# Kernel optimization log

Measured on AMD Instinct MI355X. Metric: run time of the kernel, lower is better.

Reference implementation:

```python
import jax, jax.numpy as jnp
import numpy as np

BATCH = 1048576
D_IN = 4        # d_in=3 spatial dims + 1 time dim
HID = 64
N_HID_STACK = 4  # hidden residual blocks after the first hidden layer
D_OUT = 3
BN_EPS = 1e-5


def _bn(x, gamma, beta):
    # BatchNorm1d in training mode: biased batch statistics over the batch axis
    mu = jnp.mean(x, axis=0)
    var = jnp.var(x, axis=0)
    return gamma * (x - mu) * jax.lax.rsqrt(var + BN_EPS) + beta


def setup_inputs() -> dict:
    key = jax.random.key(0)
    ks = jax.random.split(key, 8)
    s_in = 1.0 / np.sqrt(D_IN)
    s_h = 1.0 / np.sqrt(HID)
    return {
        "x": jax.random.normal(ks[0], (BATCH, D_IN), dtype=jnp.float32),
        "bn0_gamma": jnp.ones((D_IN,), jnp.float32),
        "bn0_beta": jnp.zeros((D_IN,), jnp.float32),
        "W0": jax.random.normal(ks[1], (D_IN, HID), jnp.float32) * s_in,
        "b0": jnp.zeros((HID,), jnp.float32),
        "gamma0": jnp.ones((HID,), jnp.float32),
        "beta0": jnp.zeros((HID,), jnp.float32),
        "W_hid": jax.random.normal(ks[2], (N_HID_STACK, HID, HID), jnp.float32) * s_h,
        "b_hid": jnp.zeros((N_HID_STACK, HID), jnp.float32),
        "gamma_hid": jnp.ones((N_HID_STACK, HID), jnp.float32),
        "beta_hid": jnp.zeros((N_HID_STACK, HID), jnp.float32),
        "Wout": jax.random.normal(ks[3], (HID, D_OUT), jnp.float32) * s_h,
        "bout": jnp.zeros((D_OUT,), jnp.float32),
    }


def reference(x, bn0_gamma, bn0_beta, W0, b0, gamma0, beta0,
              W_hid, b_hid, gamma_hid, beta_hid, Wout, bout):
    # Net.forward (u-network, single patch, batch_normalization=True, tanh):
    #   x = bn0(x)
    #   y = bn(act(Linear0(x)))                 (first hidden layer, no skip)
    #   y = bn_i(act(Linear_i(y))) + y          (residual hidden layers)
    #   y = Linear_out(y)
    h = _bn(x, bn0_gamma, bn0_beta)
    y = _bn(jnp.tanh(h @ W0 + b0), gamma0, beta0)

    def step(y, layer):
        W, b, g, be = layer
        return _bn(jnp.tanh(y @ W + b), g, be) + y, None

    y, _ = jax.lax.scan(step, y, (W_hid, b_hid, gamma_hid, beta_hid))
    return y @ Wout + bout
```

## Files before the change

kernel.cpp:

```cpp
#include <hip/hip_runtime.h>
#include <stdint.h>


#define NROWS 1048576
#define EPS 1e-5f
#define INV_B 9.5367431640625e-07f
#define LOG2E2 2.885390081777927f
#define BIGGRID 16384
#define NBUCKET 256

typedef __attribute__((ext_vector_type(8))) short bfrag;
typedef __attribute__((ext_vector_type(4))) float facc;
typedef __attribute__((ext_vector_type(4))) float f4v;

__device__ __forceinline__ float bf2f(short s) {
  union { unsigned u; float f; } v;
  v.u = ((unsigned)(unsigned short)s) << 16;
  return v.f;
}
__device__ __forceinline__ short f2bf(float f) {
  union { float f; unsigned u; } v;
  v.f = f;
  unsigned r = v.u + 0x7FFFu + ((v.u >> 16) & 1u);
  return (short)(r >> 16);
}
__device__ __forceinline__ float tanh_fast(float x) {
  float e = __builtin_amdgcn_exp2f(x * LOG2E2);
  return 1.f - 2.f * __builtin_amdgcn_rcpf(e + 1.f);
}

template <int W>
__global__ __launch_bounds__(256) void k_reduce(const float* __restrict__ P,
                                                float* __restrict__ S,
                                                int rows_per_blk) {
  __shared__ float red[256];
  const int tid = threadIdx.x;
  const int col = tid % W;
  const int grp = tid / W;
  const int G = 256 / W;
  size_t r0 = (size_t)blockIdx.x * rows_per_blk;
  float s = 0.f;
  for (int r = grp; r < rows_per_blk; r += G) s += P[(r0 + r) * W + col];
  red[tid] = s;
  __syncthreads();
  if (tid < W) {
    float t = 0.f;
#pragma unroll 4
    for (int g = 0; g < G; ++g) t += red[g * W + tid];
    atomicAdd(&S[tid], t);
  }
}


__global__ __launch_bounds__(256) void k_stats_x(const float* __restrict__ x,
                                                 float* __restrict__ P) {
  __shared__ float red[4][8];
  const int tid = threadIdx.x;
  const int wave = tid >> 6;
  size_t base = (size_t)blockIdx.x * 1024 + tid;
  float s[4] = {0.f, 0.f, 0.f, 0.f}, q[4] = {0.f, 0.f, 0.f, 0.f};
#pragma unroll
  for (int it = 0; it < 4; ++it) {
    f4v v = *(const f4v*)(x + (base + (size_t)it * 256) * 4);
#pragma unroll
    for (int k = 0; k < 4; ++k) { s[k] += v[k]; q[k] = fmaf(v[k], v[k], q[k]); }
  }
#pragma unroll
  for (int off = 32; off > 0; off >>= 1) {
#pragma unroll
    for (int k = 0; k < 4; ++k) {
      s[k] += __shfl_xor(s[k], off);
      q[k] += __shfl_xor(q[k], off);
    }
  }
  if ((tid & 63) == 0) {
#pragma unroll
    for (int k = 0; k < 4; ++k) { red[wave][k] = s[k]; red[wave][4 + k] = q[k]; }
  }
  __syncthreads();
  if (tid < 8)
    P[blockIdx.x * 8 + tid] =
        red[0][tid] + red[1][tid] + red[2][tid] + red[3][tid];
}

__global__ __launch_bounds__(256) void k_stats_z1(
    const float* __restrict__ x, const float* __restrict__ bn0g,
    const float* __restrict__ bn0b, const float* __restrict__ W0,
    const float* __restrict__ b0, const float* __restrict__ sx,
    float* __restrict__ P) {
  __shared__ float red[2][4][64];
  const int tid = threadIdx.x;
  const int lane = tid & 63;
  const int wave = tid >> 6;
  int gw = blockIdx.x * 4 + wave;
  float sc[4], sh[4];
#pragma unroll
  for (int k = 0; k < 4; ++k) {
    float mean = sx[k] * INV_B;
    float var = fmaf(-mean, mean, sx[4 + k] * INV_B);
    float rs = rsqrtf(var + EPS);
    sc[k] = bn0g[k] * rs;
    sh[k] = fmaf(-sc[k], mean, bn0b[k]);
  }
  float w2[4];
  float b2 = b0[lane];
#pragma unroll
  for (int k = 0; k < 4; ++k) {
    float w = W0[k * 64 + lane];
    w2[k] = sc[k] * w;
    b2 = fmaf(sh[k], w, b2);
  }
  float s = 0.f, q = 0.f;
  size_t r0 = (size_t)gw * 256;
  for (int r = 0; r < 256; ++r) {
    f4v xv = *(const f4v*)(x + (r0 + r) * 4);
    float acc = b2;
#pragma unroll
    for (int k = 0; k < 4; ++k) acc = fmaf(xv[k], w2[k], acc);
    float z = tanh_fast(acc);
    s += z;
    q = fmaf(z, z, q);
  }
  red[0][wave][lane] = s;
  red[1][wave][lane] = q;
  __syncthreads();
  if (tid < 128) {
    int which = tid >> 6, c = tid & 63;
    P[blockIdx.x * 128 + tid] = red[which][0][c] + red[which][1][c] +
                                red[which][2][c] + red[which][3][c];
  }
}

__global__ __launch_bounds__(256) void k_prep(const float* __restrict__ Wh,
                                              short* __restrict__ WT) {
  int idx = blockIdx.x * 256 + threadIdx.x;
  int l = idx >> 12, rem = idx & 4095, k = rem >> 6, c = rem & 63;
  WT[l * 4096 + c * 64 + k] = f2bf(Wh[l * 4096 + k * 64 + c]);
}


__global__ __launch_bounds__(128) void k_first(
    const float* __restrict__ x, const float* __restrict__ bn0g,
    const float* __restrict__ bn0b, const float* __restrict__ W0,
    const float* __restrict__ b0, const float* __restrict__ gamma0,
    const float* __restrict__ beta0, const float* __restrict__ sx,
    const float* __restrict__ s1, const short* __restrict__ WTb,
    const float* __restrict__ bb, float* __restrict__ Pb,
    short* __restrict__ Y) {
  __shared__ __align__(16) float lds_x[64 * 4];
  __shared__ __align__(16) short lds_y[64 * 72];
  __shared__ float lds_st[128];

  const int tid = threadIdx.x;
  const int lane = tid & 63;
  const int wave = tid >> 6;
  const int l15 = lane & 15;
  const int q = lane >> 4;
  const int wr = wave * 32;
  const size_t r0 = (size_t)blockIdx.x * 64;

  f4v xp;
  if (lane < 32) xp = *(const f4v*)(x + (r0 + wr + lane) * 4);

  lds_st[tid] = 0.f;
  float sc0[4], sh0[4];
#pragma unroll
  for (int k = 0; k < 4; ++k) {
    float mean = sx[k] * INV_B;
    float var = fmaf(-mean, mean, sx[4 + k] * INV_B);
    float rs = rsqrtf(var + EPS);
    sc0[k] = bn0g[k] * rs;
    sh0[k] = fmaf(-sc0[k], mean, bn0b[k]);
  }
  float w2[4];
  float b2 = b0[lane];
#pragma unroll
  for (int k = 0; k < 4; ++k) {
    float w = W0[k * 64 + lane];
    w2[k] = sc0[k] * w;
    b2 = fmaf(sh0[k], w, b2);
  }
  float mean1 = s1[lane] * INV_B;
  float var1 = fmaf(-mean1, mean1, s1[64 + lane] * INV_B);
  float A1c = gamma0[lane] * rsqrtf(var1 + EPS);
  float B1c = fmaf(-A1c, mean1, beta0[lane]);
  if (lane < 32) *(f4v*)&lds_x[(wr + lane) * 4] = xp;
  __syncthreads();

  for (int e = 0; e < 32; ++e) {
    int row = wr + e;
    f4v xv = *(const f4v*)&lds_x[row * 4];
    float acc = b2;
#pragma unroll
    for (int k = 0; k < 4; ++k) acc = fmaf(xv[k], w2[k], acc);
    float z = tanh_fast(acc);
    lds_y[row * 72 + lane] = f2bf(fmaf(A1c, z, B1c));
  }

  bfrag af[2][2];
#pragma unroll
  for (int mt = 0; mt < 2; ++mt)
#pragma unroll
    for (int kt = 0; kt < 2; ++kt) {
      af[mt][kt] =
          *(const bfrag*)&lds_y[(wr + mt * 16 + l15) * 72 + kt * 32 + q * 8];
      *(bfrag*)(Y + (r0 + wr + mt * 16 + l15) * 64 + kt * 32 + q * 8) =
          af[mt][kt];
    }
  float bbv[4];
  bfrag bwb[4][2];
#pragma unroll
  for (int nt = 0; nt < 4; ++nt) {
    bbv[nt] = bb[nt * 16 + l15];
#pragma unroll
    for (int kt = 0; kt < 2; ++kt)
      bwb[nt][kt] =
          *(const bfrag*)(WTb + (nt * 16 + l15) * 64 + kt * 32 + q * 8);
  }
  facc acc2[2][4];
#pragma unroll
  for (int mt = 0; mt < 2; ++mt)
#pragma unroll
    for (int nt = 0; nt < 4; ++nt) {
      acc2[mt][nt][0] = bbv[nt]; acc2[mt][nt][1] = bbv[nt];
      acc2[mt][nt][2] = bbv[nt]; acc2[mt][nt][3] = bbv[nt];
    }
#pragma unroll
  for (int mt = 0; mt < 2; ++mt)
#pragma unroll
    for (int nt = 0; nt < 4; ++nt)
#pragma unroll
      for (int kt = 0; kt < 2; ++kt)
        acc2[mt][nt] = __builtin_amdgcn_mfma_f32_16x16x32_bf16(
            af[mt][kt], bwb[nt][kt], acc2[mt][nt], 0, 0, 0);
  float sAcc[4], qAcc[4];
#pragma unroll
  for (int nt = 0; nt < 4; ++nt) {
    sAcc[nt] = 0.f;
    qAcc[nt] = 0.f;
#pragma unroll
    for (int mt = 0; mt < 2; ++mt)
#pragma unroll
      for (int i = 0; i < 4; ++i) {
        float z = tanh_fast(acc2[mt][nt][i]);
        sAcc[nt] += z;
        qAcc[nt] = fmaf(z, z, qAcc[nt]);
      }
    float s = sAcc[nt], ss = qAcc[nt];
    s += __shfl_xor(s, 16); s += __shfl_xor(s, 32);
    ss += __shfl_xor(ss, 16); ss += __shfl_xor(ss, 32);
    if (q == 0) {
      atomicAdd(&lds_st[nt * 16 + l15], s);
      atomicAdd(&lds_st[64 + nt * 16 + l15], ss);
    }
  }
  __syncthreads();
  atomicAdd(&Pb[(size_t)(blockIdx.x & (NBUCKET - 1)) * 128 + tid],
            lds_st[tid]);
}

__global__ __launch_bounds__(128) void k_mid(
    short* __restrict__ Y, const short* __restrict__ WTa,
    const float* __restrict__ ba, const float* __restrict__ ga,
    const float* __restrict__ bea, const float* __restrict__ sa,
    const short* __restrict__ WTb, const float* __restrict__ bb,
    float* __restrict__ Pb) {
  __shared__ __align__(16) short lds_y[64 * 72];
  __shared__ float red[2][128];

  const int tid = threadIdx.x;
  const int lane = tid & 63;
  const int wave = tid >> 6;
  const int l15 = lane & 15;
  const int q = lane >> 4;
  const int wr = wave * 32;
  const size_t r0 = (size_t)blockIdx.x * 64;

  bfrag af[2][2];
#pragma unroll
  for (int mt = 0; mt < 2; ++mt)
#pragma unroll
    for (int kt = 0; kt < 2; ++kt)
      af[mt][kt] =
          *(const bfrag*)(Y + (r0 + wr + mt * 16 + l15) * 64 + kt * 32 + q * 8);

  float Av[4], Bv[4], bav[4];
#pragma unroll
  for (int nt = 0; nt < 4; ++nt) {
    int c = nt * 16 + l15;
    float mean = sa[c] * INV_B;
    float var = fmaf(-mean, mean, sa[64 + c] * INV_B);
    float A = ga[c] * rsqrtf(var + EPS);
    Av[nt] = A;
    Bv[nt] = fmaf(-A, mean, bea[c]);
    bav[nt] = ba[c];
  }
  bfrag bwa[4][2];
#pragma unroll
  for (int nt = 0; nt < 4; ++nt)
#pragma unroll
    for (int kt = 0; kt < 2; ++kt)
      bwa[nt][kt] =
          *(const bfrag*)(WTa + (nt * 16 + l15) * 64 + kt * 32 + q * 8);

#pragma unroll
  for (int mt = 0; mt < 2; ++mt)
#pragma unroll
    for (int kt = 0; kt < 2; ++kt)
      *(bfrag*)&lds_y[(wr + mt * 16 + l15) * 72 + kt * 32 + q * 8] =
          af[mt][kt];

  facc acc[2][4];
#pragma unroll
  for (int mt = 0; mt < 2; ++mt)
#pragma unroll
    for (int nt = 0; nt < 4; ++nt) {
      acc[mt][nt][0] = bav[nt]; acc[mt][nt][1] = bav[nt];
      acc[mt][nt][2] = bav[nt]; acc[mt][nt][3] = bav[nt];
    }
#pragma unroll
  for (int mt = 0; mt < 2; ++mt)
#pragma unroll
    for (int nt = 0; nt < 4; ++nt)
#pragma unroll
      for (int kt = 0; kt < 2; ++kt)
        acc[mt][nt] = __builtin_amdgcn_mfma_f32_16x16x32_bf16(
            af[mt][kt], bwa[nt][kt], acc[mt][nt], 0, 0, 0);

#pragma unroll
  for (int mt = 0; mt < 2; ++mt)
#pragma unroll
    for (int nt = 0; nt < 4; ++nt) {
      int c = nt * 16 + l15;
      float A = Av[nt], Bc = Bv[nt];
#pragma unroll
      for (int i = 0; i < 4; ++i) {
        int rl = wr + mt * 16 + q * 4 + i;
        float z = tanh_fast(acc[mt][nt][i]);
        float yo = bf2f(lds_y[rl * 72 + c]);
        lds_y[rl * 72 + c] = f2bf(fmaf(A, z, Bc) + yo);
      }
    }

#pragma unroll
  for (int mt = 0; mt < 2; ++mt)
#pragma unroll
    for (int kt = 0; kt < 2; ++kt) {
      af[mt][kt] =
          *(const bfrag*)&lds_y[(wr + mt * 16 + l15) * 72 + kt * 32 + q * 8];
      *(bfrag*)(Y + (r0 + wr + mt * 16 + l15) * 64 + kt * 32 + q * 8) =
          af[mt][kt];
    }
  float bbv[4];
  bfrag bwb[4][2];
#pragma unroll
  for (int nt = 0; nt < 4; ++nt) {
    bbv[nt] = bb[nt * 16 + l15];
#pragma unroll
    for (int kt = 0; kt < 2; ++kt)
      bwb[nt][kt] =
          *(const bfrag*)(WTb + (nt * 16 + l15) * 64 + kt * 32 + q * 8);
  }
#pragma unroll
  for (int mt = 0; mt < 2; ++mt)
#pragma unroll
    for (int nt = 0; nt < 4; ++nt) {
      acc[mt][nt][0] = bbv[nt]; acc[mt][nt][1] = bbv[nt];
      acc[mt][nt][2] = bbv[nt]; acc[mt][nt][3] = bbv[nt];
    }
#pragma unroll
  for (int mt = 0; mt < 2; ++mt)
#pragma unroll
    for (int nt = 0; nt < 4; ++nt)
#pragma unroll
      for (int kt = 0; kt < 2; ++kt)
        acc[mt][nt] = __builtin_amdgcn_mfma_f32_16x16x32_bf16(
            af[mt][kt], bwb[nt][kt], acc[mt][nt], 0, 0, 0);
#pragma unroll
  for (int nt = 0; nt < 4; ++nt) {
    float s = 0.f, ss = 0.f;
#pragma unroll
    for (int mt = 0; mt < 2; ++mt)
#pragma unroll
      for (int i = 0; i < 4; ++i) {
        float z = tanh_fast(acc[mt][nt][i]);
        s += z;
        ss = fmaf(z, z, ss);
      }
    s += __shfl_xor(s, 16); s += __shfl_xor(s, 32);
    ss += __shfl_xor(ss, 16); ss += __shfl_xor(ss, 32);
    if (q == 0) {
      red[wave][nt * 16 + l15] = s;
      red[wave][64 + nt * 16 + l15] = ss;
    }
  }
  __syncthreads();
  atomicAdd(&Pb[(size_t)(blockIdx.x & (NBUCKET - 1)) * 128 + tid],
            red[0][tid] + red[1][tid]);
}

__global__ __launch_bounds__(128) void k_last(
    const short* __restrict__ Y, const short* __restrict__ WTa,
    const float* __restrict__ ba, const float* __restrict__ ga,
    const float* __restrict__ bea, const float* __restrict__ sa,
    const float* __restrict__ Wout, const float* __restrict__ bout,
    float* __restrict__ out) {
  __shared__ __align__(16) short lds_y[64 * 72];
  __shared__ float lds_wo[192];

  const int tid = threadIdx.x;
  const int lane = tid & 63;
  const int wave = tid >> 6;
  const int l15 = lane & 15;
  const int q = lane >> 4;
  const int wr = wave * 32;
  const size_t r0 = (size_t)blockIdx.x * 64;

  bfrag af[2][2];
#pragma unroll
  for (int mt = 0; mt < 2; ++mt)
#pragma unroll
    for (int kt = 0; kt < 2; ++kt)
      af[mt][kt] =
          *(const bfrag*)(Y + (r0 + wr + mt * 16 + l15) * 64 + kt * 32 + q * 8);

  for (int i = tid; i < 192; i += 128) lds_wo[i] = Wout[i];
  float Av[4], Bv[4], bav[4];
#pragma unroll
  for (int nt = 0; nt < 4; ++nt) {
    int c = nt * 16 + l15;
    float mean = sa[c] * INV_B;
    float var = fmaf(-mean, mean, sa[64 + c] * INV_B);
    float A = ga[c] * rsqrtf(var + EPS);
    Av[nt] = A;
    Bv[nt] = fmaf(-A, mean, bea[c]);
    bav[nt] = ba[c];
  }
  bfrag bwa[4][2];
#pragma unroll
  for (int nt = 0; nt < 4; ++nt)
#pragma unroll
    for (int kt = 0; kt < 2; ++kt)
      bwa[nt][kt] =
          *(const bfrag*)(WTa + (nt * 16 + l15) * 64 + kt * 32 + q * 8);
  float bo0 = bout[0], bo1 = bout[1], bo2 = bout[2];

#pragma unroll
  for (int mt = 0; mt < 2; ++mt)
#pragma unroll
    for (int kt = 0; kt < 2; ++kt)
      *(bfrag*)&lds_y[(wr + mt * 16 + l15) * 72 + kt * 32 + q * 8] =
          af[mt][kt];
  __syncthreads();

  facc acc[2][4];
#pragma unroll
  for (int mt = 0; mt < 2; ++mt)
#pragma unroll
    for (int nt = 0; nt < 4; ++nt) {
      acc[mt][nt][0] = bav[nt]; acc[mt][nt][1] = bav[nt];
      acc[mt][nt][2] = bav[nt]; acc[mt][nt][3] = bav[nt];
    }
#pragma unroll
  for (int mt = 0; mt < 2; ++mt)
#pragma unroll
    for (int nt = 0; nt < 4; ++nt)
#pragma unroll
      for (int kt = 0; kt < 2; ++kt)
        acc[mt][nt] = __builtin_amdgcn_mfma_f32_16x16x32_bf16(
            af[mt][kt], bwa[nt][kt], acc[mt][nt], 0, 0, 0);
#pragma unroll
  for (int mt = 0; mt < 2; ++mt)
#pragma unroll
    for (int nt = 0; nt < 4; ++nt) {
      int c = nt * 16 + l15;
      float A = Av[nt], Bc = Bv[nt];
#pragma unroll
      for (int i = 0; i < 4; ++i) {
        int rl = wr + mt * 16 + q * 4 + i;
        float z = tanh_fast(acc[mt][nt][i]);
        float yo = bf2f(lds_y[rl * 72 + c]);
        lds_y[rl * 72 + c] = f2bf(fmaf(A, z, Bc) + yo);
      }
    }

  {
    int row = wr + (lane >> 1);
    int cb = (lane & 1) * 32;
    float o0 = 0.f, o1 = 0.f, o2 = 0.f;
#pragma unroll
    for (int jc = 0; jc < 4; ++jc) {
      bfrag v = *(const bfrag*)&lds_y[row * 72 + cb + jc * 8];
#pragma unroll
      for (int j = 0; j < 8; ++j) {
        float f = bf2f(v[j]);
        int jj = cb + jc * 8 + j;
        o0 = fmaf(f, lds_wo[jj * 3 + 0], o0);
        o1 = fmaf(f, lds_wo[jj * 3 + 1], o1);
        o2 = fmaf(f, lds_wo[jj * 3 + 2], o2);
      }
    }
    o0 += __shfl_xor(o0, 1);
    o1 += __shfl_xor(o1, 1);
    o2 += __shfl_xor(o2, 1);
    if ((lane & 1) == 0) {
      size_t ro = (r0 + row) * 3;
      out[ro] = o0 + bo0;
      out[ro + 1] = o1 + bo1;
      out[ro + 2] = o2 + bo2;
    }
  }
}

extern "C" void kernel_launch(void* const* d_in, const int* in_sizes, int n_in,
                              void* d_out, int out_size, void* d_ws,
                              size_t ws_size, hipStream_t stream) {
  (void)in_sizes; (void)n_in; (void)out_size; (void)ws_size;
  const float* x = (const float*)d_in[0];
  const float* bn0g = (const float*)d_in[1];
  const float* bn0b = (const float*)d_in[2];
  const float* W0 = (const float*)d_in[3];
  const float* b0 = (const float*)d_in[4];
  const float* gamma0 = (const float*)d_in[5];
  const float* beta0 = (const float*)d_in[6];
  const float* Wh = (const float*)d_in[7];
  const float* bh = (const float*)d_in[8];
  const float* gh = (const float*)d_in[9];
  const float* beh = (const float*)d_in[10];
  const float* Wout = (const float*)d_in[11];
  const float* bout = (const float*)d_in[12];
  float* out = (float*)d_out;

  char* ws = (char*)d_ws;
  short* Y = (short*)ws;
  const size_t YB = (size_t)NROWS * 64 * 2;
  float* stats = (float*)(ws + YB);
  float* Sx = stats;
  float* S1 = stats + 8;
  float* S2 = stats + 136;
  float* S3 = stats + 264;
  float* S4 = stats + 392;
  float* S5 = stats + 520;
  short* WT = (short*)(ws + YB + 4096);
  float* P = (float*)(ws + YB + 4096 + 32768);
  float* Pb = (float*)(ws + YB + 4096 + 32768 + (1 << 20));
  float* Pb2 = Pb;
  float* Pb3 = Pb + NBUCKET * 128;
  float* Pb4 = Pb + 2 * NBUCKET * 128;
  float* Pb5 = Pb + 3 * NBUCKET * 128;

  hipMemsetAsync(stats, 0, 648 * sizeof(float), stream);
  hipMemsetAsync(Pb, 0, 4 * NBUCKET * 128 * sizeof(float), stream);
  k_prep<<<64, 256, 0, stream>>>(Wh, WT);
  k_stats_x<<<1024, 256, 0, stream>>>(x, P);
  k_reduce<8><<<8, 256, 0, stream>>>(P, Sx, 128);
  k_stats_z1<<<1024, 256, 0, stream>>>(x, bn0g, bn0b, W0, b0, Sx, P);
  k_reduce<128><<<8, 256, 0, stream>>>(P, S1, 128);
  k_first<<<BIGGRID, 128, 0, stream>>>(x, bn0g, bn0b, W0, b0, gamma0, beta0,
                                       Sx, S1, WT, bh, Pb2, Y);
  k_reduce<128><<<16, 256, 0, stream>>>(Pb2, S2, 16);
  k_mid<<<BIGGRID, 128, 0, stream>>>(Y, WT, bh, gh, beh, S2, WT + 4096,
                                     bh + 64, Pb3);
  k_reduce<128><<<16, 256, 0, stream>>>(Pb3, S3, 16);
  k_mid<<<BIGGRID, 128, 0, stream>>>(Y, WT + 4096, bh + 64, gh + 64, beh + 64,
                                     S3, WT + 2 * 4096, bh + 128, Pb4);
  k_reduce<128><<<16, 256, 0, stream>>>(Pb4, S4, 16);
  k_mid<<<BIGGRID, 128, 0, stream>>>(Y, WT + 2 * 4096, bh + 128, gh + 128,
                                     beh + 128, S4, WT + 3 * 4096, bh + 192,
                                     Pb5);
  k_reduce<128><<<16, 256, 0, stream>>>(Pb5, S5, 16);
  k_last<<<BIGGRID, 128, 0, stream>>>(Y, WT + 3 * 4096, bh + 192, gh + 192,
                                      beh + 192, S5, Wout, bout, out);
}
```

Baseline: 534.3 us.

## Use hardware packed bf16 conversion, coalesce Y loads, replace LDS atomics with per-wave partials

Swaps the software round-to-nearest bf16 conversion for the packed v_cvt_pk_bf16_f32 instruction in the first, mid and last kernels. k_mid and k_last now load Y with row-contiguous coalesced 16-byte accesses and stage them through LDS before reading the MFMA fragments, instead of gathering fragments directly from global memory. k_first replaces LDS atomicAdd statistics with per-wave partial arrays summed at the end, and drops one __syncthreads. The added LDS staging costs extra LDS traffic, and removing the sync in k_first relies on each wave only reading the lds_x rows it wrote itself.

```diff
diff --git a/kernel.cpp b/kernel.cpp
--- a/kernel.cpp
+++ b/kernel.cpp
@@ -23,6 +23,11 @@
   v.f = f;
   unsigned r = v.u + 0x7FFFu + ((v.u >> 16) & 1u);
   return (short)(r >> 16);
+}
+__device__ __forceinline__ unsigned cvt_pk_bf16(float lo, float hi) {
+  unsigned r;
+  asm("v_cvt_pk_bf16_f32 %0, %1, %2" : "=v"(r) : "v"(lo), "v"(hi));
+  return r;
 }
 __device__ __forceinline__ float tanh_fast(float x) {
   float e = __builtin_amdgcn_exp2f(x * LOG2E2);
@@ -149,7 +154,7 @@
     short* __restrict__ Y) {
   __shared__ __align__(16) float lds_x[64 * 4];
   __shared__ __align__(16) short lds_y[64 * 72];
-  __shared__ float lds_st[128];
+  __shared__ float red[2][128];
 
   const int tid = threadIdx.x;
   const int lane = tid & 63;
@@ -162,7 +167,6 @@
   f4v xp;
   if (lane < 32) xp = *(const f4v*)(x + (r0 + wr + lane) * 4);
 
-  lds_st[tid] = 0.f;
   float sc0[4], sh0[4];
 #pragma unroll
   for (int k = 0; k < 4; ++k) {
@@ -185,16 +189,21 @@
   float A1c = gamma0[lane] * rsqrtf(var1 + EPS);
   float B1c = fmaf(-A1c, mean1, beta0[lane]);
   if (lane < 32) *(f4v*)&lds_x[(wr + lane) * 4] = xp;
-  __syncthreads();
-
-  for (int e = 0; e < 32; ++e) {
+
+  for (int e = 0; e < 32; e += 2) {
     int row = wr + e;
-    f4v xv = *(const f4v*)&lds_x[row * 4];
-    float acc = b2;
-#pragma unroll
-    for (int k = 0; k < 4; ++k) acc = fmaf(xv[k], w2[k], acc);
-    float z = tanh_fast(acc);
-    lds_y[row * 72 + lane] = f2bf(fmaf(A1c, z, B1c));
+    f4v xv0 = *(const f4v*)&lds_x[row * 4];
+    f4v xv1 = *(const f4v*)&lds_x[(row + 1) * 4];
+    float a0 = b2, a1 = b2;
+#pragma unroll
+    for (int k = 0; k < 4; ++k) {
+      a0 = fmaf(xv0[k], w2[k], a0);
+      a1 = fmaf(xv1[k], w2[k], a1);
+    }
+    float z0 = tanh_fast(a0), z1 = tanh_fast(a1);
+    unsigned p = cvt_pk_bf16(fmaf(A1c, z0, B1c), fmaf(A1c, z1, B1c));
+    lds_y[row * 72 + lane] = (short)p;
+    lds_y[(row + 1) * 72 + lane] = (short)(p >> 16);
   }
 
   bfrag af[2][2];
@@ -233,30 +242,27 @@
       for (int kt = 0; kt < 2; ++kt)
         acc2[mt][nt] = __builtin_amdgcn_mfma_f32_16x16x32_bf16(
             af[mt][kt], bwb[nt][kt], acc2[mt][nt], 0, 0, 0);
-  float sAcc[4], qAcc[4];
 #pragma unroll
   for (int nt = 0; nt < 4; ++nt) {
-    sAcc[nt] = 0.f;
-    qAcc[nt] = 0.f;
+    float s = 0.f, ss = 0.f;
 #pragma unroll
     for (int mt = 0; mt < 2; ++mt)
 #pragma unroll
       for (int i = 0; i < 4; ++i) {
         float z = tanh_fast(acc2[mt][nt][i]);
-        sAcc[nt] += z;
-        qAcc[nt] = fmaf(z, z, qAcc[nt]);
+        s += z;
+        ss = fmaf(z, z, ss);
       }
-    float s = sAcc[nt], ss = qAcc[nt];
     s += __shfl_xor(s, 16); s += __shfl_xor(s, 32);
     ss += __shfl_xor(ss, 16); ss += __shfl_xor(ss, 32);
     if (q == 0) {
-      atomicAdd(&lds_st[nt * 16 + l15], s);
-      atomicAdd(&lds_st[64 + nt * 16 + l15], ss);
+      red[wave][nt * 16 + l15] = s;
+      red[wave][64 + nt * 16 + l15] = ss;
     }
   }
   __syncthreads();
   atomicAdd(&Pb[(size_t)(blockIdx.x & (NBUCKET - 1)) * 128 + tid],
-            lds_st[tid]);
+            red[0][tid] + red[1][tid]);
 }
 
 __global__ __launch_bounds__(128) void k_mid(
@@ -275,14 +281,16 @@
   const int q = lane >> 4;
   const int wr = wave * 32;
   const size_t r0 = (size_t)blockIdx.x * 64;
-
-  bfrag af[2][2];
-#pragma unroll
-  for (int mt = 0; mt < 2; ++mt)
-#pragma unroll
-    for (int kt = 0; kt < 2; ++kt)
-      af[mt][kt] =
-          *(const bfrag*)(Y + (r0 + wr + mt * 16 + l15) * 64 + kt * 32 + q * 8);
+  const int srow = lane >> 3;
+  const int sc8 = (lane & 7) * 8;
+
+  bfrag ld[4];
+  {
+    const size_t g = (r0 + wr + srow) * 64 + sc8;
+#pragma unroll
+    for (int it = 0; it < 4; ++it)
+      ld[it] = *(const bfrag*)(Y + g + (size_t)it * 8 * 64);
+  }
 
   float Av[4], Bv[4], bav[4];
 #pragma unroll
@@ -304,12 +312,16 @@
           *(const bfrag*)(WTa + (nt * 16 + l15) * 64 + kt * 32 + q * 8);
 
 #pragma unroll
+  for (int it = 0; it < 4; ++it)
+    *(bfrag*)&lds_y[(wr + it * 8 + srow) * 72 + sc8] = ld[it];
+
+  bfrag af[2][2];
+#pragma unroll
   for (int mt = 0; mt < 2; ++mt)
 #pragma unroll
     for (int kt = 0; kt < 2; ++kt)
-      *(bfrag*)&lds_y[(wr + mt * 16 + l15) * 72 + kt * 32 + q * 8] =
-          af[mt][kt];
-
+      af[mt][kt] =
+          *(const bfrag*)&lds_y[(wr + mt * 16 + l15) * 72 + kt * 32 + q * 8];
   facc acc[2][4];
 #pragma unroll
   for (int mt = 0; mt < 2; ++mt)
@@ -333,13 +345,21 @@
     for (int nt = 0; nt < 4; ++nt) {
       int c = nt * 16 + l15;
       float A = Av[nt], Bc = Bv[nt];
-#pragma unroll
-      for (int i = 0; i < 4; ++i) {
-        int rl = wr + mt * 16 + q * 4 + i;
-        float z = tanh_fast(acc[mt][nt][i]);
-        float yo = bf2f(lds_y[rl * 72 + c]);
-        lds_y[rl * 72 + c] = f2bf(fmaf(A, z, Bc) + yo);
-      }
+      int rb = wr + mt * 16 + q * 4;
+      float v0 = fmaf(A, tanh_fast(acc[mt][nt][0]), Bc) +
+                 bf2f(lds_y[(rb + 0) * 72 + c]);
+      float v1 = fmaf(A, tanh_fast(acc[mt][nt][1]), Bc) +
+                 bf2f(lds_y[(rb + 1) * 72 + c]);
+      float v2 = fmaf(A, tanh_fast(acc[mt][nt][2]), Bc) +
+                 bf2f(lds_y[(rb + 2) * 72 + c]);
+      float v3 = fmaf(A, tanh_fast(acc[mt][nt][3]), Bc) +
+                 bf2f(lds_y[(rb + 3) * 72 + c]);
+      unsigned p01 = cvt_pk_bf16(v0, v1);
+      unsigned p23 = cvt_pk_bf16(v2, v3);
+      lds_y[(rb + 0) * 72 + c] = (short)p01;
+      lds_y[(rb + 1) * 72 + c] = (short)(p01 >> 16);
+      lds_y[(rb + 2) * 72 + c] = (short)p23;
+      lds_y[(rb + 3) * 72 + c] = (short)(p23 >> 16);
     }
 
 #pragma unroll
@@ -415,14 +435,16 @@
   const int q = lane >> 4;
   const int wr = wave * 32;
   const size_t r0 = (size_t)blockIdx.x * 64;
-
-  bfrag af[2][2];
-#pragma unroll
-  for (int mt = 0; mt < 2; ++mt)
-#pragma unroll
-    for (int kt = 0; kt < 2; ++kt)
-      af[mt][kt] =
-          *(const bfrag*)(Y + (r0 + wr + mt * 16 + l15) * 64 + kt * 32 + q * 8);
+  const int srow = lane >> 3;
+  const int sc8 = (lane & 7) * 8;
+
+  bfrag ld[4];
+  {
+    const size_t g = (r0 + wr + srow) * 64 + sc8;
+#pragma unroll
+    for (int it = 0; it < 4; ++it)
+      ld[it] = *(const bfrag*)(Y + g + (size_t)it * 8 * 64);
+  }
 
   for (int i = tid; i < 192; i += 128) lds_wo[i] = Wout[i];
   float Av[4], Bv[4], bav[4];
@@ -446,13 +468,17 @@
   float bo0 = bout[0], bo1 = bout[1], bo2 = bout[2];
 
 #pragma unroll
+  for (int it = 0; it < 4; ++it)
+    *(bfrag*)&lds_y[(wr + it * 8 + srow) * 72 + sc8] = ld[it];
+  __syncthreads();
+
+  bfrag af[2][2];
+#pragma unroll
   for (int mt = 0; mt < 2; ++mt)
 #pragma unroll
     for (int kt = 0; kt < 2; ++kt)
-      *(bfrag*)&lds_y[(wr + mt * 16 + l15) * 72 + kt * 32 + q * 8] =
-          af[mt][kt];
-  __syncthreads();
-
+      af[mt][kt] =
+          *(const bfrag*)&lds_y[(wr + mt * 16 + l15) * 72 + kt * 32 + q * 8];
   facc acc[2][4];
 #pragma unroll
   for (int mt = 0; mt < 2; ++mt)
@@ -475,13 +501,21 @@
     for (int nt = 0; nt < 4; ++nt) {
       int c = nt * 16 + l15;
       float A = Av[nt], Bc = Bv[nt];
-#pragma unroll
-      for (int i = 0; i < 4; ++i) {
-        int rl = wr + mt * 16 + q * 4 + i;
-        float z = tanh_fast(acc[mt][nt][i]);
-        float yo = bf2f(lds_y[rl * 72 + c]);
-        lds_y[rl * 72 + c] = f2bf(fmaf(A, z, Bc) + yo);
-      }
+      int rb = wr + mt * 16 + q * 4;
+      float v0 = fmaf(A, tanh_fast(acc[mt][nt][0]), Bc) +
+                 bf2f(lds_y[(rb + 0) * 72 + c]);
+      float v1 = fmaf(A, tanh_fast(acc[mt][nt][1]), Bc) +
+                 bf2f(lds_y[(rb + 1) * 72 + c]);
+      float v2 = fmaf(A, tanh_fast(acc[mt][nt][2]), Bc) +
+                 bf2f(lds_y[(rb + 2) * 72 + c]);
+      float v3 = fmaf(A, tanh_fast(acc[mt][nt][3]), Bc) +
+                 bf2f(lds_y[(rb + 3) * 72 + c]);
+      unsigned p01 = cvt_pk_bf16(v0, v1);
+      unsigned p23 = cvt_pk_bf16(v2, v3);
+      lds_y[(rb + 0) * 72 + c] = (short)p01;
+      lds_y[(rb + 1) * 72 + c] = (short)(p01 >> 16);
+      lds_y[(rb + 2) * 72 + c] = (short)p23;
+      lds_y[(rb + 3) * 72 + c] = (short)(p23 >> 16);
     }
 
   {
```

After: 490.9 us. -8.1%, faster.
